# Optimization experiments

Measured on AMD Instinct MI355X. Metric: run time of the kernel, lower is better.

## Reference

```python
import jax, jax.numpy as jnp
import numpy as np

EMBED = 896
HQ = 16      # query heads
HK = 4       # kv heads
D = EMBED // HQ          # 56 head dim
KV_EMBED = D * HK        # 224
G = HQ // HK             # 4 groups per kv head
LN_EPS = 1e-5


def setup_inputs() -> dict:
    key = jax.random.key(0)
    ks = jax.random.split(key, 8)
    b, n = 2, 2048
    inp = {
        "query": jax.random.normal(ks[0], (b, n, EMBED), jnp.float32),
        "key":   jax.random.normal(ks[1], (b, n, EMBED), jnp.float32),
        "value": jax.random.normal(ks[2], (b, n, EMBED), jnp.float32),
        # torch Linear weights are (out_features, in_features), y = x @ W.T
        "Wq": jax.random.normal(ks[3], (EMBED, EMBED), jnp.float32) * 0.02,
        "Wk": jax.random.normal(ks[4], (KV_EMBED, EMBED), jnp.float32) * 0.02,
        "Wv": jax.random.normal(ks[5], (KV_EMBED, EMBED), jnp.float32) * 0.02,
        "Wo": jax.random.normal(ks[6], (EMBED, EMBED), jnp.float32) * 0.02,
        "ln_gamma": jnp.ones((EMBED,), jnp.float32),
        "ln_beta": jnp.zeros((EMBED,), jnp.float32),
    }
    return inp


def _layer_norm(x, gamma, beta):
    mu = jnp.mean(x, axis=-1, keepdims=True)
    var = jnp.var(x, axis=-1, keepdims=True)
    return (x - mu) * jax.lax.rsqrt(var + LN_EPS) * gamma + beta


def reference(query, key, value, Wq, Wk, Wv, Wo, ln_gamma, ln_beta):
    b, n, _ = query.shape
    s = key.shape[1]
    # projections
    q = query @ Wq.T                      # (b, n, EMBED)
    k = key @ Wk.T                        # (b, s, KV_EMBED)
    v = value @ Wv.T                      # (b, s, KV_EMBED)
    # split heads: q -> (b, hk, g, n, d); k, v -> (b, hk, s, d)
    q = q.reshape(b, n, HQ, D).transpose(0, 2, 1, 3)      # (b, hq, n, d)
    q = q.reshape(b, HK, G, n, D)                          # (b, hk, g, n, d)
    k = k.reshape(b, s, HK, D).transpose(0, 2, 1, 3)       # (b, hk, s, d)
    v = v.reshape(b, s, HK, D).transpose(0, 2, 1, 3)       # (b, hk, s, d)
    # scaled scores
    scale = jnp.asarray(D, q.dtype) ** 0.5
    scores = jnp.einsum('bhgnd,bhsd->bhgns', q, k) / scale  # (b, hk, g, n, s)
    # causal mask
    mask = jnp.tril(jnp.ones((n, s), bool))                # (n, s)
    scores = jnp.where(mask, scores, jnp.asarray(-jnp.inf, scores.dtype))
    attn = jax.nn.softmax(scores, axis=-1)                 # (b, hk, g, n, s)
    # (dropout is identity in deterministic eval-mode reference)
    out = jnp.einsum('bhgns,bhsd->bhgnd', attn, v)         # (b, hk, g, n, d)
    # merge heads back: (h g) ordering matches the query split
    out = out.transpose(0, 3, 1, 2, 4).reshape(b, n, EMBED)  # b n (h g d)
    out = _layer_norm(out, ln_gamma, ln_beta)
    out = out @ Wo.T                                        # (b, n, EMBED)
    # need_weights + average_attn_weights: b h g n s -> b n s (h g), mean over n
    aw = attn.transpose(0, 3, 4, 1, 2).reshape(b, n, s, HQ).mean(axis=1)  # (b, s, hq)
    return out, aw
```

## Files before the change

### kernel.cpp

```cpp
#include <hip/hip_runtime.h>

#define B_    2
#define N_    2048
#define EMBED 896
#define HQ    16
#define HK    4
#define D_    56
#define DP    64

typedef unsigned short u16;
typedef unsigned int   u32;
typedef __attribute__((ext_vector_type(8))) short bf16x8;
typedef __attribute__((ext_vector_type(4))) float f32x4;

__device__ __forceinline__ u16 f2bf(float f) {
  u32 u = __builtin_bit_cast(u32, f);
  return (u16)((u + 0x7FFFu + ((u >> 16) & 1u)) >> 16);
}

__device__ __forceinline__ float bf2f(u16 x) {
  u32 u = (u32)x << 16;
  return __builtin_bit_cast(float, u);
}

__device__ __forceinline__ u32 cvtpk_bf16(float lo, float hi) {
  u32 r;
  asm("v_cvt_pk_bf16_f32 %0, %1, %2" : "=v"(r) : "v"(lo), "v"(hi));
  return r;
}

#define EXP2F(x) __builtin_amdgcn_exp2f(x)

__device__ __forceinline__ void gload_lds16(const u16* g, u16* l) {
  __builtin_amdgcn_global_load_lds(
      (const __attribute__((address_space(1))) void*)g,
      (__attribute__((address_space(3))) void*)l, 16, 0, 0);
}

#define QSCALE 0.19278822f

__global__ __launch_bounds__(256) void pad_zero(u16* __restrict__ Qp,
                                                u16* __restrict__ Kp,
                                                u16* __restrict__ Vt) {
  int i = blockIdx.x * 256 + threadIdx.x;
  int4 z = {0, 0, 0, 0};
  if (i < 65536) {
    *(int4*)(Qp + (size_t)i * 64 + 56) = z;
  } else if (i < 81920) {
    *(int4*)(Kp + (size_t)(i - 65536) * 64 + 56) = z;
  } else {
    int j = i - 81920;
    int bhk = j >> 11;
    int off = j & 2047;
    *(int4*)(Vt + ((size_t)bhk * 64 + 56) * 2048 + (size_t)off * 8) = z;
  }
}

#define SEG_IN  3670016u
#define SEG_WQ  802816u
#define SEG_WK  200704u

__global__ __launch_bounds__(256) void to_bf16(
    const float* __restrict__ q, const float* __restrict__ k,
    const float* __restrict__ v, const float* __restrict__ wq,
    const float* __restrict__ wk, const float* __restrict__ wv,
    const float* __restrict__ wo, u16* __restrict__ qb, u16* __restrict__ kb,
    u16* __restrict__ vb, u16* __restrict__ wqb, u16* __restrict__ wkb,
    u16* __restrict__ wvb, u16* __restrict__ wob) {
  size_t e = ((size_t)blockIdx.x * 256 + threadIdx.x) * 4;
  const float* src;
  u16* dst;
  size_t off;
  if (e < SEG_IN)            { src = q;  dst = qb;  off = e; }
  else if (e < 2 * (size_t)SEG_IN) { src = k;  dst = kb;  off = e - SEG_IN; }
  else if (e < 3 * (size_t)SEG_IN) { src = v;  dst = vb;  off = e - 2 * (size_t)SEG_IN; }
  else {
    size_t r = e - 3 * (size_t)SEG_IN;
    if (r < SEG_WQ)                    { src = wq; dst = wqb; off = r; }
    else if (r < SEG_WQ + SEG_WK)      { src = wk; dst = wkb; off = r - SEG_WQ; }
    else if (r < SEG_WQ + 2 * SEG_WK)  { src = wv; dst = wvb; off = r - SEG_WQ - SEG_WK; }
    else                               { src = wo; dst = wob; off = r - SEG_WQ - 2 * SEG_WK; }
  }
  float4 v4 = *(const float4*)(src + off);
  uint2 pb;
  pb.x = (u32)f2bf(v4.x) | ((u32)f2bf(v4.y) << 16);
  pb.y = (u32)f2bf(v4.z) | ((u32)f2bf(v4.w) << 16);
  *(uint2*)(dst + off) = pb;
}

#define NT_K 14

#define GEMM_CORE(APTR, WPTR)                                                  \
  for (int it = 0; it < NT_K; ++it) {                                          \
    const int k0 = it * 64;                                                    \
    {                                                                          \
      const u16* Ag = (APTR) + (size_t)m0 * EMBED + k0;                        \
      _Pragma("unroll") for (int i = 0; i < 4; i++) {                          \
        int f = i * 256 + t;                                                   \
        int r = f >> 3, s = (f & 7) ^ (r & 7);                                 \
        gload_lds16(Ag + (size_t)r * EMBED + s * 8,                            \
                    AsL + (i * 256 + fwbase) * 8);                             \
      }                                                                        \
      const u16* Wg = (WPTR) + (size_t)wn0 * EMBED + k0;                       \
      _Pragma("unroll") for (int i = 0; i < 2; i++) {                          \
        int f = i * 256 + t;                                                   \
        int r = f >> 3, s = (f & 7) ^ (r & 7);                                 \
        gload_lds16(Wg + (size_t)r * EMBED + s * 8,                            \
                    BsL + (i * 256 + fwbase) * 8);                             \
      }                                                                        \
    }                                                                          \
    __syncthreads();                  \
    _Pragma("unroll") for (int kk = 0; kk < 2; kk++) {                         \
      bf16x8 af[2], bfv[4];                                                    \
      _Pragma("unroll") for (int mf = 0; mf < 2; mf++) {                       \
        int ra = wr + mf * 16 + fr;                                            \
        af[mf] =                                                               \
            *(const bf16x8*)&AsL[ra * 64 + ((fg + kk * 4) ^ (ra & 7)) * 8];    \
      }                                                                        \
      _Pragma("unroll") for (int nf = 0; nf < 4; nf++) {                       \
        int rb = nf * 16 + fr;                                                 \
        bfv[nf] =                                                              \
            *(const bf16x8*)&BsL[rb * 64 + ((fg + kk * 4) ^ (rb & 7)) * 8];    \
      }                                                                        \
      _Pragma("unroll") for (int mf = 0; mf < 2; mf++)                         \
          _Pragma("unroll") for (int nf = 0; nf < 4; nf++)                     \
              acc[mf][nf] = __builtin_amdgcn_mfma_f32_16x16x32_bf16(           \
                  af[mf], bfv[nf], acc[mf][nf], 0, 0, 0);                      \
    }                                                                          \
    __syncthreads();        \
  }

__global__ __launch_bounds__(256) void proj_gemm(
    const u16* __restrict__ qb, const u16* __restrict__ kb,
    const u16* __restrict__ vb, const u16* __restrict__ Wqb,
    const u16* __restrict__ Wkb, const u16* __restrict__ Wvb,
    u16* __restrict__ Qp, u16* __restrict__ Kp, u16* __restrict__ Vt) {
  __shared__ __align__(16) u16 lds[12288];
  u16* AsL = lds;
  u16* BsL = lds + 8192;
  const int t = threadIdx.x;
  const int m0 = blockIdx.x * 128;
  const int y = blockIdx.y;
  int p, nt;
  if (y < 14)      { p = 0; nt = y; }
  else if (y < 18) { p = 1; nt = y - 14; }
  else             { p = 2; nt = y - 18; }
  const u16* A = p == 0 ? qb : (p == 1 ? kb : vb);
  const u16* W = p == 0 ? Wqb : (p == 1 ? Wkb : Wvb);
  const int Nproj = p == 0 ? 896 : 224;
  const int wn0 = nt * 64;

  const int w = t >> 6, lane = t & 63;
  const int fr = lane & 15, fg = lane >> 4;
  const int wr = w * 32;
  const int fwbase = t & 192;

  f32x4 acc[2][4] = {};

  GEMM_CORE(A, W)

  if (p < 2) {
#pragma unroll
    for (int nf = 0; nf < 4; nf++) {
      int col = wn0 + nf * 16 + fr;
      if (col < Nproj) {
        int hh = col / 56, d = col - hh * 56;
#pragma unroll
        for (int mf = 0; mf < 2; mf++)
#pragma unroll
          for (int r = 0; r < 4; r++) {
            int row = m0 + wr + mf * 16 + fg * 4 + r;
            int bb = row >> 11, nn = row & 2047;
            float vv = acc[mf][nf][r];
            if (p == 0)
              Qp[((size_t)((bb * 16 + hh) * 2048 + nn)) * 64 + d] =
                  f2bf(vv * QSCALE);
            else
              Kp[((size_t)((bb * 4 + hh) * 2048 + nn)) * 64 + d] = f2bf(vv);
          }
      }
    }
  } else {
    u16* Traw = lds;
#define TS(r_, c_) Traw[(r_)*136 + (c_)]
#pragma unroll
    for (int nf = 0; nf < 4; nf++)
#pragma unroll
      for (int mf = 0; mf < 2; mf++)
#pragma unroll
        for (int r = 0; r < 4; r++)
          TS(nf * 16 + fr, wr + mf * 16 + fg * 4 + r) = f2bf(acc[mf][nf][r]);
    __syncthreads();
    const int bb = m0 >> 11, n_base = m0 & 2047;
#pragma unroll
    for (int i = 0; i < 4; i++) {
      int flat = i * 256 + t;
      int dr = flat >> 4;
      int c8 = (flat & 15) * 8;
      int col = wn0 + dr;
      if (col < 224) {
        int hh = col / 56, d = col - hh * 56;
        *(int4*)(Vt + ((size_t)((bb * 4 + hh) * 64 + d)) * 2048 + n_base + c8) =
            *(int4*)&TS(dr, c8);
      }
    }
  }
}

__global__ __launch_bounds__(256) void gemm_wo(const u16* __restrict__ A,
                                               const u16* __restrict__ W,
                                               float* __restrict__ C) {
  __shared__ __align__(16) u16 lds[12288];
  u16* AsL = lds;
  u16* BsL = lds + 8192;
  const int t = threadIdx.x;
  const int m0 = blockIdx.x * 128;
  const int wn0 = blockIdx.y * 64;
  const int w = t >> 6, lane = t & 63;
  const int fr = lane & 15, fg = lane >> 4;
  const int wr = w * 32;
  const int fwbase = t & 192;

  f32x4 acc[2][4] = {};

  GEMM_CORE(A, W)

#pragma unroll
  for (int nf = 0; nf < 4; nf++) {
    int col = wn0 + nf * 16 + fr;
#pragma unroll
    for (int mf = 0; mf < 2; mf++)
#pragma unroll
      for (int r = 0; r < 4; r++) {
        int row = m0 + wr + mf * 16 + fg * 4 + r;
        C[(size_t)row * EMBED + col] = acc[mf][nf][r];
      }
  }
}

__global__ __launch_bounds__(256) void repack_qf(const u16* __restrict__ Qp,
                                                 u16* __restrict__ Qf) {
  const int tile = blockIdx.x;
  const u16* src = Qp + (size_t)tile * 4096;
  u16* dst = Qf + (size_t)tile * 4096;
  __shared__ __align__(16) u16 T[4096];
  const int t = threadIdx.x;
#pragma unroll
  for (int i = 0; i < 2; i++) {
    int f = i * 256 + t;
    int r = f >> 3, c8 = f & 7;
    *(int4*)&T[(r * 8 + (c8 ^ (r & 7))) * 8] = *(const int4*)(src + f * 8);
  }
  __syncthreads();
#pragma unroll
  for (int i = 0; i < 2; i++) {
    int f = i * 256 + t;
    int fr = f & 15, fg = (f >> 4) & 3, kk = (f >> 6) & 1, ifr = (f >> 7) & 3;
    int row = ifr * 16 + fr, c8 = (kk * 32 + fg * 8) >> 3;
    *(int4*)(dst + f * 8) = *(int4*)&T[(row * 8 + (c8 ^ (row & 7))) * 8];
  }
}

__global__ __launch_bounds__(256) void attn_fwd(const u16* __restrict__ Qp,
                                                const u16* __restrict__ Kp,
                                                const u16* __restrict__ Vt,
                                                u16* __restrict__ Op,
                                                float* __restrict__ lp) {
  const int p = blockIdx.x, hk = blockIdx.y;
  const int b = blockIdx.z >> 1, sg = blockIdx.z & 1;
  const int t = threadIdx.x, w = t >> 6, lane = t & 63;
  const int fr = lane & 15, fg = lane >> 4;
  const int h = hk * 4 + w;

  __shared__ __align__(16) u16 KVs[2][2][4096];
  __shared__ __align__(16) u16 Ps[4 * 16 * 64];

  const u16* Qh = Qp + (size_t)(b * HQ + h) * N_ * DP;
  const u16* Kh = Kp + (size_t)(b * HK + hk) * N_ * DP;
  const u16* Vh = Vt + (size_t)(b * HK + hk) * DP * N_;

  const int fwb = t & 192;
  const int fx = fr & 7;

#define PSW(w_, row_, col8_) ((w_)*1024 + (row_)*64 + (((col8_) ^ ((row_)&7)) * 8))

#define ISSUE_KV(ntt_, buf_)                                                   \
  do {                                                                         \
    const u16* Kb = Kh + (size_t)(ntt_)*64 * DP;                               \
    const u16* Vb = Vh + (ntt_)*64;                                            \
    _Pragma("unroll") for (int i = 0; i < 2; i++) {                            \
      int f = i * 256 + t;                                                     \
      int r = f >> 3, sl = (f & 7) ^ (r & 7);                                  \
      gload_lds16(Kb + (size_t)r * DP + sl * 8,                                \
                  &KVs[buf_][0][(i * 256 + fwb) * 8]);                         \
      gload_lds16(Vb + (size_t)r * N_ + sl * 8,                                \
                  &KVs[buf_][1][(i * 256 + fwb) * 8]);                         \
    }                                                                          \
  } while (0)

  const int s0 = p, s1 = 127 - p;
  const int ntf0 = (s0 >> 2) + 1, ntf1 = (s1 >> 2) + 1;
  const int lo0 = sg ? (ntf0 >> 1) : 0, hi0 = sg ? ntf0 : (ntf0 >> 1);
  const int lo1 = sg ? (ntf1 >> 1) : 0, hi1 = sg ? ntf1 : (ntf1 >> 1);

  int bi = 0;
  if (hi0 > lo0) {
    ISSUE_KV(lo0, 0);
  } else if (hi1 > lo1) {
    ISSUE_KV(lo1, 0);
  }

  for (int half = 0; half < 2; ++half) {
    const int s = half ? s1 : s0;
    const int ntf = half ? ntf1 : ntf0;
    const int lo = half ? lo1 : lo0, hi = half ? hi1 : hi0;

    bf16x8 qf[2];
#pragma unroll
    for (int kk = 0; kk < 2; kk++)
      qf[kk] = *(const bf16x8*)(Qh + (size_t)(s * 16 + fr) * DP +
                                kk * 32 + fg * 8);

    f32x4 oacc[4] = {};
    float l_acc[4] = {};

    for (int tt = lo; tt < hi; ++tt) {
      __syncthreads();
      {
        int ntt = -1;
        if (tt + 1 < hi) ntt = tt + 1;
        else if (half == 0 && hi1 > lo1) ntt = lo1;
        if (ntt >= 0) {
          ISSUE_KV(ntt, bi ^ 1);
        }
      }

      f32x4 sacc[4] = {};
#pragma unroll
      for (int kk = 0; kk < 2; kk++) {
        bf16x8 bk[4];
#pragma unroll
        for (int jf = 0; jf < 4; jf++)
          bk[jf] = *(const bf16x8*)&KVs[bi][0][(jf * 16 + fr) * 64 +
                                               ((kk * 4 + fg) ^ fx) * 8];
#pragma unroll
        for (int jf = 0; jf < 4; jf++)
          sacc[jf] = __builtin_amdgcn_mfma_f32_16x16x32_bf16(
              qf[kk], bk[jf], sacc[jf], 0, 0, 0);
      }

      if (tt == ntf - 1) {
#pragma unroll
        for (int jf = 0; jf < 4; jf++) {
          int gj = tt * 64 + jf * 16 + fr;
          float pv[4];
#pragma unroll
          for (int r = 0; r < 4; r++) {
            int gi = s * 16 + fg * 4 + r;
            pv[r] = (gj <= gi) ? EXP2F(sacc[jf][r]) : 0.f;
            l_acc[r] += pv[r];
          }
          u32 w01 = cvtpk_bf16(pv[0], pv[1]);
          u32 w23 = cvtpk_bf16(pv[2], pv[3]);
          int c8 = jf * 2 + (fr >> 3), c7 = fr & 7;
          Ps[PSW(w, fg * 4 + 0, c8) + c7] = (u16)w01;
          Ps[PSW(w, fg * 4 + 1, c8) + c7] = (u16)(w01 >> 16);
          Ps[PSW(w, fg * 4 + 2, c8) + c7] = (u16)w23;
          Ps[PSW(w, fg * 4 + 3, c8) + c7] = (u16)(w23 >> 16);
        }
      } else {
#pragma unroll
        for (int jf = 0; jf < 4; jf++) {
          float pv[4];
#pragma unroll
          for (int r = 0; r < 4; r++) {
            pv[r] = EXP2F(sacc[jf][r]);
            l_acc[r] += pv[r];
          }
          u32 w01 = cvtpk_bf16(pv[0], pv[1]);
          u32 w23 = cvtpk_bf16(pv[2], pv[3]);
          int c8 = jf * 2 + (fr >> 3), c7 = fr & 7;
          Ps[PSW(w, fg * 4 + 0, c8) + c7] = (u16)w01;
          Ps[PSW(w, fg * 4 + 1, c8) + c7] = (u16)(w01 >> 16);
          Ps[PSW(w, fg * 4 + 2, c8) + c7] = (u16)w23;
          Ps[PSW(w, fg * 4 + 3, c8) + c7] = (u16)(w23 >> 16);
        }
      }

#pragma unroll
      for (int kk = 0; kk < 2; kk++) {
        bf16x8 ap = *(const bf16x8*)&Ps[PSW(w, fr, kk * 4 + fg)];
        bf16x8 bv[4];
#pragma unroll
        for (int df = 0; df < 4; df++)
          bv[df] = *(const bf16x8*)&KVs[bi][1][(df * 16 + fr) * 64 +
                                               ((kk * 4 + fg) ^ fx) * 8];
#pragma unroll
        for (int df = 0; df < 4; df++)
          oacc[df] = __builtin_amdgcn_mfma_f32_16x16x32_bf16(
              ap, bv[df], oacc[df], 0, 0, 0);
      }
      bi ^= 1;
    }

#pragma unroll
    for (int r = 0; r < 4; r++) {
      float v = l_acc[r];
      v += __shfl_xor(v, 1);
      v += __shfl_xor(v, 2);
      v += __shfl_xor(v, 4);
      v += __shfl_xor(v, 8);
      l_acc[r] = v;
    }
    const size_t obase = (((size_t)(sg * 2 + b) * 16 + h) * 2048 + s * 16);
#pragma unroll
    for (int df = 0; df < 4; df++) {
      int d = df * 16 + fr;
      if (d < D_) {
#pragma unroll
        for (int r = 0; r < 4; r++)
          Op[(obase + fg * 4 + r) * 56 + d] = f2bf(oacc[df][r]);
      }
    }
    if (fr == 0) {
#pragma unroll
      for (int r = 0; r < 4; r++)
        lp[obase + fg * 4 + r] = l_acc[r];
    }
  }
}

struct QTile {
  bf16x8 q[4][2];
  float li[4];
};

#define LOADQ(dst, rt_)                                                        \
  {                                                                            \
    _Pragma("unroll") for (int ifr = 0; ifr < 4; ifr++) {                      \
      _Pragma("unroll") for (int kk = 0; kk < 2; kk++)                         \
          dst.q[ifr][kk] = *(const bf16x8*)(Qfh +                              \
              ((((size_t)(rt_)*4 + ifr) * 2 + kk) * 64 + fg * 16 + fr) * 8);   \
      dst.li[ifr] = linv_h[(rt_)*64 + ifr * 16 + fr];                          \
    }                                                                          \
  }

#define COMPUTET(src, rt_)                                                     \
  {                                                                            \
    f32x4 tacc[2][4] = {};                                                     \
    _Pragma("unroll") for (int kk = 0; kk < 2; kk++)                           \
        _Pragma("unroll") for (int jm = 0; jm < 2; jm++)                       \
        _Pragma("unroll") for (int ifr = 0; ifr < 4; ifr++)                    \
            tacc[jm][ifr] = __builtin_amdgcn_mfma_f32_16x16x32_bf16(           \
                kf[jm][kk], src.q[ifr][kk], tacc[jm][ifr], 0, 0, 0);           \
    if ((rt_) == rt0) {                                                        \
      _Pragma("unroll") for (int jm = 0; jm < 2; jm++)                         \
          _Pragma("unroll") for (int ifr = 0; ifr < 4; ifr++)                  \
          _Pragma("unroll") for (int r = 0; r < 4; r++) {                      \
        int gi = (rt_)*64 + ifr * 16 + fr;                                     \
        int gj = ct * 32 + jm * 16 + fg * 4 + r;                               \
        if (gi >= gj)                                                          \
          s_acc[jm][r] += EXP2F(tacc[jm][ifr][r]) * src.li[ifr];               \
      }                                                                        \
    } else {                                                                   \
      _Pragma("unroll") for (int jm = 0; jm < 2; jm++)                         \
          _Pragma("unroll") for (int ifr = 0; ifr < 4; ifr++)                  \
          _Pragma("unroll") for (int r = 0; r < 4; r++)                        \
              s_acc[jm][r] += EXP2F(tacc[jm][ifr][r]) * src.li[ifr];           \
    }                                                                          \
  }

__global__ __launch_bounds__(256) void attn_aw(const u16* __restrict__ Qf,
                                               const u16* __restrict__ Kp,
                                               const float* __restrict__ linv_g,
                                               float* __restrict__ aw) {
  const int bid = blockIdx.x;
  const int xcd = bid & 7, idx = bid >> 3;
  const int g = xcd + 8 * (idx >> 5);
  const int p = idx & 31;
  const int b = g >> 4, h = g & 15;
  const int hk = h >> 2;
  const int t = threadIdx.x, w = t >> 6, lane = t & 63;
  const int fr = lane & 15, fg = lane >> 4;

  __shared__ float red[2][4][32];

  const u16* Qfh = Qf + (size_t)(b * HQ + h) * N_ * DP;
  const u16* Kh = Kp + (size_t)(b * HK + hk) * N_ * DP;
  const float* linv_h = linv_g + (size_t)(b * HQ + h) * N_;

  for (int half = 0; half < 2; ++half) {
    const int ct = half ? (63 - p) : p;
    const int rt0 = ct >> 1;

    bf16x8 kf[2][2];
#pragma unroll
    for (int jm = 0; jm < 2; jm++)
#pragma unroll
      for (int kk = 0; kk < 2; kk++)
        kf[jm][kk] = *(const bf16x8*)(Kh + (size_t)(ct * 32 + jm * 16 + fr) * DP +
                                      kk * 32 + fg * 8);

    float s_acc[2][4] = {};
    QTile qa, qb;
    int rt = rt0 + w;
    if (rt <= 31) {
      LOADQ(qa, rt);
      while (true) {
        if (rt + 4 <= 31) LOADQ(qb, rt + 4);
        COMPUTET(qa, rt);
        rt += 4;
        if (rt > 31) break;
        if (rt + 4 <= 31) LOADQ(qa, rt + 4);
        COMPUTET(qb, rt);
        rt += 4;
        if (rt > 31) break;
      }
    }

#pragma unroll
    for (int jm = 0; jm < 2; jm++)
#pragma unroll
      for (int r = 0; r < 4; r++) {
        float v = s_acc[jm][r];
        v += __shfl_xor(v, 1);
        v += __shfl_xor(v, 2);
        v += __shfl_xor(v, 4);
        v += __shfl_xor(v, 8);
        if (fr == 0) red[half][w][jm * 16 + fg * 4 + r] = v;
      }
  }

  __syncthreads();
  if (w == 0 && fr == 0) {
#pragma unroll
    for (int half = 0; half < 2; ++half) {
      const int ct = half ? (63 - p) : p;
#pragma unroll
      for (int jm = 0; jm < 2; jm++)
#pragma unroll
        for (int r = 0; r < 4; r++) {
          int idx2 = jm * 16 + fg * 4 + r;
          float v = red[half][0][idx2] + red[half][1][idx2] +
                    red[half][2][idx2] + red[half][3][idx2];
          int gj = ct * 32 + jm * 16 + fg * 4 + r;
          aw[((size_t)b * N_ + gj) * HQ + h] = v * (1.0f / N_);
        }
    }
  }
}

__global__ __launch_bounds__(256) void ln_fwd(const u16* __restrict__ Op,
                                              const float* __restrict__ lp,
                                              const float* __restrict__ gamma,
                                              const float* __restrict__ beta,
                                              u16* __restrict__ out,
                                              float* __restrict__ linv_g) {
  const int row = blockIdx.x;
  const int b = row >> 11, n = row & 2047;
  const int t = threadIdx.x;
  __shared__ float lrec[16];
  __shared__ float red[8];

  if (t < 16) {
    float l0 = lp[((size_t)(0 + b) * 16 + t) * 2048 + n];
    float l1 = lp[((size_t)(2 + b) * 16 + t) * 2048 + n];
    float ri = 1.0f / (l0 + l1);
    lrec[t] = ri;
    linv_g[((size_t)b * 16 + t) * 2048 + n] = ri;
  }
  __syncthreads();

  float s = 0.f, s2 = 0.f;
  float v[4];
#pragma unroll
  for (int i = 0; i < 4; i++) {
    int c = t + 256 * i;
    if (c < EMBED) {
      int h = c / 56, d = c - h * 56;
      size_t o0 = (((size_t)(0 + b) * 16 + h) * 2048 + n) * 56 + d;
      size_t o1 = (((size_t)(2 + b) * 16 + h) * 2048 + n) * 56 + d;
      v[i] = (bf2f(Op[o0]) + bf2f(Op[o1])) * lrec[h];
    } else {
      v[i] = 0.f;
    }
    s += v[i];
    s2 += v[i] * v[i];
  }
#pragma unroll
  for (int m = 1; m <= 32; m <<= 1) {
    s += __shfl_xor(s, m);
    s2 += __shfl_xor(s2, m);
  }
  const int w = t >> 6, lane = t & 63;
  if (lane == 0) {
    red[w] = s;
    red[4 + w] = s2;
  }
  __syncthreads();
  s = red[0] + red[1] + red[2] + red[3];
  s2 = red[4] + red[5] + red[6] + red[7];
  const float mu = s * (1.0f / EMBED);
  const float var = s2 * (1.0f / EMBED) - mu * mu;
  const float rs = rsqrtf(var + 1e-5f);
#pragma unroll
  for (int i = 0; i < 4; i++) {
    int c = t + 256 * i;
    if (c < EMBED)
      out[(size_t)row * EMBED + c] = f2bf((v[i] - mu) * rs * gamma[c] + beta[c]);
  }
}

extern "C" void kernel_launch(void* const* d_in, const int* in_sizes, int n_in,
                              void* d_out, int out_size, void* d_ws,
                              size_t ws_size, hipStream_t stream) {
  (void)in_sizes; (void)n_in; (void)out_size; (void)ws_size;
  const float* query = (const float*)d_in[0];
  const float* key   = (const float*)d_in[1];
  const float* value = (const float*)d_in[2];
  const float* Wq    = (const float*)d_in[3];
  const float* Wk    = (const float*)d_in[4];
  const float* Wv    = (const float*)d_in[5];
  const float* Wo    = (const float*)d_in[6];
  const float* gamma = (const float*)d_in[7];
  const float* beta  = (const float*)d_in[8];

  float* out = (float*)d_out;
  float* aw  = out + (size_t)B_ * N_ * EMBED;

  char* ws = (char*)d_ws;
  u16* Qp = (u16*)ws;        ws += (size_t)B_ * HQ * N_ * DP * 2;
  u16* Kp = (u16*)ws;        ws += (size_t)B_ * HK * N_ * DP * 2;
  u16* Vt = (u16*)ws;        ws += (size_t)B_ * HK * N_ * DP * 2;
  u16* Qf = (u16*)ws;        ws += (size_t)B_ * HQ * N_ * DP * 2;
  float* linv = (float*)ws;  ws += (size_t)B_ * HQ * N_ * 4;
  float* lp   = (float*)ws;  ws += (size_t)4 * HQ * N_ * 4;
  u16* Wqb = (u16*)ws;       ws += (size_t)SEG_WQ * 2;
  u16* Wkb = (u16*)ws;       ws += (size_t)SEG_WK * 2;
  u16* Wvb = (u16*)ws;       ws += (size_t)SEG_WK * 2;
  u16* Wob = (u16*)ws;       ws += (size_t)SEG_WQ * 2;
  char* region = ws;
  u16* qb = (u16*)region;
  u16* kb = qb + (size_t)SEG_IN;
  u16* vb = kb + (size_t)SEG_IN;
  u16* Op  = (u16*)region;
  u16* LNo = Op + (size_t)4 * HQ * N_ * 56;

  dim3 blk(256);
  const int M = B_ * N_;

  pad_zero<<<dim3(384), blk, 0, stream>>>(Qp, Kp, Vt);

  to_bf16<<<dim3(12712), blk, 0, stream>>>(query, key, value, Wq, Wk, Wv, Wo,
                                           qb, kb, vb, Wqb, Wkb, Wvb, Wob);

  proj_gemm<<<dim3(M / 128, 22), blk, 0, stream>>>(qb, kb, vb, Wqb, Wkb, Wvb,
                                                   Qp, Kp, Vt);

  repack_qf<<<dim3(B_ * HQ * (N_ / 64)), blk, 0, stream>>>(Qp, Qf);

  attn_fwd<<<dim3(64, HK, B_ * 2), blk, 0, stream>>>(Qp, Kp, Vt, Op, lp);
  ln_fwd<<<dim3(M), blk, 0, stream>>>(Op, lp, gamma, beta, LNo, linv);

  attn_aw<<<dim3(1024), blk, 0, stream>>>(Qf, Kp, linv, aw);
  gemm_wo<<<dim3(M / 128, 14), blk, 0, stream>>>(LNo, Wob, out);
}
```

Baseline: 128.0 us.

## Keep softmax probabilities in registers by computing transposed scores for PV MFMA

Swaps the QK^T MFMA operands so each lane holds a score column laid out to match the A-operand of the 16x16x16 bf16 MFMA. The P tile can then feed the PV product straight from registers instead of round-tripping through shared memory. The PV step uses 16x16x16 MFMAs with 4-element V loads, and the row-sum reduction now shuffles across lane groups. This removes the LDS writes and reads of P and their bank traffic, at the cost of twice as many smaller MFMA instructions and narrower V reads.

Measured after the change: 122.8 us. 1.04x faster.

```diff
diff --git a/kernel.cpp b/kernel.cpp
--- a/kernel.cpp
+++ b/kernel.cpp
@@ -11,6 +11,7 @@
 typedef unsigned short u16;
 typedef unsigned int   u32;
 typedef __attribute__((ext_vector_type(8))) short bf16x8;
+typedef __attribute__((ext_vector_type(4))) short bf16x4;
 typedef __attribute__((ext_vector_type(4))) float f32x4;
 
 __device__ __forceinline__ u16 f2bf(float f) {
@@ -273,7 +274,6 @@
   const int h = hk * 4 + w;
 
   __shared__ __align__(16) u16 KVs[2][2][4096];
-  __shared__ __align__(16) u16 Ps[4 * 16 * 64];
 
   const u16* Qh = Qp + (size_t)(b * HQ + h) * N_ * DP;
   const u16* Kh = Kp + (size_t)(b * HK + hk) * N_ * DP;
@@ -281,8 +281,6 @@
 
   const int fwb = t & 192;
   const int fx = fr & 7;
-
-#define PSW(w_, row_, col8_) ((w_)*1024 + (row_)*64 + (((col8_) ^ ((row_)&7)) * 8))
 
 #define ISSUE_KV(ntt_, buf_)                                                   \
   do {                                                                         \
@@ -322,7 +320,7 @@
                                 kk * 32 + fg * 8);
 
     f32x4 oacc[4] = {};
-    float l_acc[4] = {};
+    float l_lane = 0.f;
 
     for (int tt = lo; tt < hi; ++tt) {
       __syncthreads();
@@ -346,27 +344,23 @@
 #pragma unroll
         for (int jf = 0; jf < 4; jf++)
           sacc[jf] = __builtin_amdgcn_mfma_f32_16x16x32_bf16(
-              qf[kk], bk[jf], sacc[jf], 0, 0, 0);
-      }
-
+              bk[jf], qf[kk], sacc[jf], 0, 0, 0);
+      }
+
+      bf16x4 pa[4];
       if (tt == ntf - 1) {
+        const int gi = s * 16 + fr;
 #pragma unroll
         for (int jf = 0; jf < 4; jf++) {
-          int gj = tt * 64 + jf * 16 + fr;
           float pv[4];
 #pragma unroll
           for (int r = 0; r < 4; r++) {
-            int gi = s * 16 + fg * 4 + r;
+            int gj = tt * 64 + jf * 16 + fg * 4 + r;
             pv[r] = (gj <= gi) ? EXP2F(sacc[jf][r]) : 0.f;
-            l_acc[r] += pv[r];
+            l_lane += pv[r];
           }
-          u32 w01 = cvtpk_bf16(pv[0], pv[1]);
-          u32 w23 = cvtpk_bf16(pv[2], pv[3]);
-          int c8 = jf * 2 + (fr >> 3), c7 = fr & 7;
-          Ps[PSW(w, fg * 4 + 0, c8) + c7] = (u16)w01;
-          Ps[PSW(w, fg * 4 + 1, c8) + c7] = (u16)(w01 >> 16);
-          Ps[PSW(w, fg * 4 + 2, c8) + c7] = (u16)w23;
-          Ps[PSW(w, fg * 4 + 3, c8) + c7] = (u16)(w23 >> 16);
+          uint2 pk = {cvtpk_bf16(pv[0], pv[1]), cvtpk_bf16(pv[2], pv[3])};
+          pa[jf] = __builtin_bit_cast(bf16x4, pk);
         }
       } else {
 #pragma unroll
@@ -375,58 +369,45 @@
 #pragma unroll
           for (int r = 0; r < 4; r++) {
             pv[r] = EXP2F(sacc[jf][r]);
-            l_acc[r] += pv[r];
+            l_lane += pv[r];
           }
-          u32 w01 = cvtpk_bf16(pv[0], pv[1]);
-          u32 w23 = cvtpk_bf16(pv[2], pv[3]);
-          int c8 = jf * 2 + (fr >> 3), c7 = fr & 7;
-          Ps[PSW(w, fg * 4 + 0, c8) + c7] = (u16)w01;
-          Ps[PSW(w, fg * 4 + 1, c8) + c7] = (u16)(w01 >> 16);
-          Ps[PSW(w, fg * 4 + 2, c8) + c7] = (u16)w23;
-          Ps[PSW(w, fg * 4 + 3, c8) + c7] = (u16)(w23 >> 16);
+          uint2 pk = {cvtpk_bf16(pv[0], pv[1]), cvtpk_bf16(pv[2], pv[3])};
+          pa[jf] = __builtin_bit_cast(bf16x4, pk);
         }
       }
 
 #pragma unroll
-      for (int kk = 0; kk < 2; kk++) {
-        bf16x8 ap = *(const bf16x8*)&Ps[PSW(w, fr, kk * 4 + fg)];
-        bf16x8 bv[4];
-#pragma unroll
-        for (int df = 0; df < 4; df++)
-          bv[df] = *(const bf16x8*)&KVs[bi][1][(df * 16 + fr) * 64 +
-                                               ((kk * 4 + fg) ^ fx) * 8];
-#pragma unroll
-        for (int df = 0; df < 4; df++)
-          oacc[df] = __builtin_amdgcn_mfma_f32_16x16x32_bf16(
-              ap, bv[df], oacc[df], 0, 0, 0);
+      for (int df = 0; df < 4; df++) {
+        const int vrow = (df * 16 + fr) * 64;
+#pragma unroll
+        for (int jf = 0; jf < 4; jf++) {
+          bf16x4 bv = *(const bf16x4*)&KVs[bi][1][vrow +
+                                                  (((jf * 2 + (fg >> 1)) ^ fx) * 8) +
+                                                  (fg & 1) * 4];
+          oacc[df] = __builtin_amdgcn_mfma_f32_16x16x16bf16_1k(
+              pa[jf], bv, oacc[df], 0, 0, 0);
+        }
       }
       bi ^= 1;
     }
 
-#pragma unroll
-    for (int r = 0; r < 4; r++) {
-      float v = l_acc[r];
-      v += __shfl_xor(v, 1);
-      v += __shfl_xor(v, 2);
-      v += __shfl_xor(v, 4);
-      v += __shfl_xor(v, 8);
-      l_acc[r] = v;
+    {
+      float v = l_lane;
+      v += __shfl_xor(v, 16);
+      v += __shfl_xor(v, 32);
+      const size_t obase = (((size_t)(sg * 2 + b) * 16 + h) * 2048 + s * 16);
+      if (fg == 0) lp[obase + fr] = v;
+#pragma unroll
+      for (int df = 0; df < 4; df++) {
+        int d = df * 16 + fr;
+        if (d < D_) {
+#pragma unroll
+          for (int r = 0; r < 4; r++)
+            Op[(obase + fg * 4 + r) * 56 + d] = f2bf(oacc[df][r]);
+        }
+      }
     }
-    const size_t obase = (((size_t)(sg * 2 + b) * 16 + h) * 2048 + s * 16);
-#pragma unroll
-    for (int df = 0; df < 4; df++) {
-      int d = df * 16 + fr;
-      if (d < D_) {
-#pragma unroll
-        for (int r = 0; r < 4; r++)
-          Op[(obase + fg * 4 + r) * 56 + d] = f2bf(oacc[df][r]);
-      }
-    }
-    if (fr == 0) {
-#pragma unroll
-      for (int r = 0; r < 4; r++)
-        lp[obase + fg * 4 + r] = l_acc[r];
-    }
+    l_lane = 0.f;
   }
 }
 
```
